# Kernel tuning notes

Hardware: AMD Instinct MI355X
Metric: run time of the kernel (lower is better)

Reference implementation:

```python
import jax, jax.numpy as jnp
import numpy as np

CH = 64
SCALE = 2
GROUPS = 4
K = 3
GN_GROUPS = min(CH // 8, 8)  # = 8
EPS_GN = 1e-5
EPS_COS = 1e-8


def setup_inputs() -> dict:
    key = jax.random.key(0)
    ks = jax.random.split(key, 4)
    B, H, W = 8, 256, 256
    OC = 2 * GROUPS
    lap = jnp.array([[0., -1., 0.], [-1., 4., -1.], [0., -1., 0.]], dtype=jnp.float32)
    hp_weight = jnp.tile(lap[None, None], (CH, 1, 1, 1))  # depthwise high-pass kernel
    return {
        "x": jax.random.normal(ks[0], (B, CH, H, W), dtype=jnp.float32),
        "gn_gamma": jnp.ones((CH,), jnp.float32),
        "gn_beta": jnp.zeros((CH,), jnp.float32),
        "hp_weight": hp_weight,
        "dir_w": jax.random.normal(ks[1], (OC, K * K - 1), jnp.float32) * 0.001,
        "dir_b": jnp.zeros((OC,), jnp.float32),
        "mag_w": jax.random.normal(ks[2], (OC, CH), jnp.float32) * 0.02,
        "mag_b": jnp.zeros((OC,), jnp.float32),
        "hfg_w": jax.random.normal(ks[3], (OC, CH), jnp.float32) * 0.02,
        "hfg_b": jnp.zeros((OC,), jnp.float32),
    }


def group_norm(x, gamma, beta, g, eps=EPS_GN):
    B, C, H, W = x.shape
    xr = x.reshape(B, g, -1)
    mu = xr.mean(-1, keepdims=True)
    var = xr.var(-1, keepdims=True)
    xn = ((xr - mu) * jax.lax.rsqrt(var + eps)).reshape(B, C, H, W)
    return xn * gamma[None, :, None, None] + beta[None, :, None, None]


def dw_conv3(x, w):
    # depthwise 3x3, padding=1, no bias
    return jax.lax.conv_general_dilated(
        x, w, window_strides=(1, 1), padding=((1, 1), (1, 1)),
        dimension_numbers=("NCHW", "OIHW", "NCHW"), feature_group_count=x.shape[1])


def avg_pool(x, s):
    B, C, H, W = x.shape
    return x.reshape(B, C, H // s, s, W // s, s).mean(axis=(3, 5))


def direction_feat(x, k=K):
    # cosine similarity (over channels) of center pixel vs each of k*k neighbors, center dropped
    B, C, H, W = x.shape
    p = k // 2
    xp = jnp.pad(x, ((0, 0), (0, 0), (p, p), (p, p)))
    patches = jnp.stack([xp[:, :, i:i + H, j:j + W]
                         for i in range(k) for j in range(k)], axis=2)  # [B,C,k2,H,W]
    center = patches[:, :, k * k // 2:k * k // 2 + 1]  # [B,C,1,H,W]
    dot = (center * patches).sum(axis=1)               # [B,k2,H,W]
    n1 = jnp.sqrt((center * center).sum(axis=1))       # [B,1,H,W]
    n2 = jnp.sqrt((patches * patches).sum(axis=1))     # [B,k2,H,W]
    sim = dot / (jnp.maximum(n1, EPS_COS) * jnp.maximum(n2, EPS_COS))
    c = k * k // 2
    return jnp.concatenate([sim[:, :c], sim[:, c + 1:]], axis=1)  # [B,k2-1,H,W]


def conv1x1(w, b, x):
    return jnp.einsum("oc,bchw->bohw", w, x) + b[None, :, None, None]


def grid_sample_border(x, grid):
    # x: [N,C,H,W]; grid: [N,Hg,Wg,2] in [-1,1]; bilinear, align_corners=False, padding_mode='border'
    N, C, H, W = x.shape
    gx, gy = grid[..., 0], grid[..., 1]
    ix = jnp.clip(((gx + 1.0) * W - 1.0) * 0.5, 0.0, W - 1.0)
    iy = jnp.clip(((gy + 1.0) * H - 1.0) * 0.5, 0.0, H - 1.0)
    x0 = jnp.floor(ix); y0 = jnp.floor(iy)
    wx = (ix - x0)[..., None]; wy = (iy - y0)[..., None]
    x0i = jnp.clip(x0.astype(jnp.int32), 0, W - 1)
    y0i = jnp.clip(y0.astype(jnp.int32), 0, H - 1)
    x1i = jnp.clip(x0i + 1, 0, W - 1)
    y1i = jnp.clip(y0i + 1, 0, H - 1)
    img = x.transpose(0, 2, 3, 1)  # [N,H,W,C]
    b = jnp.arange(N)[:, None, None]
    v00 = img[b, y0i, x0i]; v01 = img[b, y0i, x1i]
    v10 = img[b, y1i, x0i]; v11 = img[b, y1i, x1i]
    out = (v00 * (1 - wx) * (1 - wy) + v01 * wx * (1 - wy)
           + v10 * (1 - wx) * wy + v11 * wx * wy)
    return out.transpose(0, 3, 1, 2)  # [N,C,Hg,Wg]


def reference(x, gn_gamma, gn_beta, hp_weight, dir_w, dir_b, mag_w, mag_b, hfg_w, hfg_b):
    B, C, H, W = x.shape
    xn = group_norm(x, gn_gamma, gn_beta, GN_GROUPS)
    hf = dw_conv3(xn, hp_weight)
    xl = avg_pool(xn, SCALE)
    hfl = avg_pool(hf, SCALE)
    df = direction_feat(xl)
    gate = jax.nn.sigmoid(conv1x1(mag_w, mag_b, xl) + conv1x1(hfg_w, hfg_b, hfl))
    offset = conv1x1(dir_w, dir_b, df) * gate  # [B, 2*GROUPS, Hl, Wl]
    Hl, Wl = H // SCALE, W // SCALE
    off = offset.reshape(B, 2, GROUPS, Hl, Wl)
    cy = jnp.arange(Hl, dtype=x.dtype) * SCALE + SCALE / 2.0  # high-res pixel centers
    cx = jnp.arange(Wl, dtype=x.dtype) * SCALE + SCALE / 2.0
    gx = (cx[None, None, None, :] + off[:, 0]) * (2.0 / W) - 1.0  # [B,G,Hl,Wl]
    gy = (cy[None, None, :, None] + off[:, 1]) * (2.0 / H) - 1.0
    grid = jnp.stack([gx, gy], axis=-1).reshape(B * GROUPS, Hl, Wl, 2)
    xg = x.reshape(B * GROUPS, C // GROUPS, H, W)
    out = grid_sample_border(xg, grid)
    return out.reshape(B, C, Hl, Wl)
```

## Files before the change

### kernel.cpp

```cpp
#include <hip/hip_runtime.h>
#include <hip/hip_bf16.h>
#include <math.h>

#define B_ 8
#define C_ 64
#define H_ 256
#define W_ 256
#define HL_ 128
#define WL_ 128
#define GN_G 8
#define CPG 8
#define GRP 4
#define OC_ 8
#define GROUP_ELEMS (CPG * H_ * W_)

#define TILE_H 16
#define XROWS 34
#define LDSW 264

__global__ __launch_bounds__(256) void k2_fused(const float* __restrict__ x,
                                                const float* __restrict__ hpw,
                                                float* __restrict__ px,
                                                float* __restrict__ pL,
                                                float* __restrict__ partials) {
  __shared__ float tile[XROWS * LDSW];
  __shared__ float rs[4], rs2[4];
  const int t = threadIdx.x;
  const int blk = blockIdx.x;
  const int tileIdx = blk & 7;
  const int bc = blk >> 3;
  const int c = bc & 63;
  const int hl0 = tileIdx * TILE_H;
  const float* plane = x + (size_t)bc * (H_ * W_);
  const int y0 = 2 * hl0 - 1;

  if (t < XROWS * 2) {
    const int r = t >> 1;
    tile[r * LDSW + ((t & 1) ? 260 : 3)] = 0.f;
  }

  float s = 0.f, s2 = 0.f;
  for (int i = 0; i < 9; ++i) {
    const int q = t + i * 256;
    if (q >= XROWS * 64) break;
    const int r = q >> 6;
    const int c4 = (q & 63) << 2;
    const int y = y0 + r;
    float4 v = make_float4(0.f, 0.f, 0.f, 0.f);
    if ((unsigned)y < (unsigned)H_)
      v = *reinterpret_cast<const float4*>(plane + y * W_ + c4);
    *reinterpret_cast<float4*>(&tile[r * LDSW + 4 + c4]) = v;
    if (r >= 1 && r <= 32) {
      s  += v.x + v.y + v.z + v.w;
      s2 += v.x * v.x + v.y * v.y + v.z * v.z + v.w * v.w;
    }
  }
#pragma unroll
  for (int off = 32; off > 0; off >>= 1) {
    s  += __shfl_down(s, off, 64);
    s2 += __shfl_down(s2, off, 64);
  }
  if ((t & 63) == 0) { rs[t >> 6] = s; rs2[t >> 6] = s2; }
  __syncthreads();
  if (t == 0) {
    partials[blk * 2 + 0] = rs[0] + rs[1] + rs[2] + rs[3];
    partials[blk * 2 + 1] = rs2[0] + rs2[1] + rs2[2] + rs2[3];
  }

  float w[9];
#pragma unroll
  for (int i = 0; i < 9; ++i) w[i] = hpw[c * 9 + i];

  const int wl = t & 127;
  const int hs = (t >> 7) * 8;
  const int colb = 3 + 2 * wl;
  const int rbase = 2 * hs;
  float win[4][4];
#pragma unroll
  for (int j = 0; j < 4; ++j)
#pragma unroll
    for (int d = 0; d < 4; ++d)
      win[j][d] = tile[(rbase + j) * LDSW + colb + d];

  int outIdx = (bc * HL_ + (hl0 + hs)) * WL_ + wl;
#pragma unroll
  for (int i = 0; i < 8; ++i) {
    float pr[4][3];
#pragma unroll
    for (int j = 0; j < 4; ++j)
#pragma unroll
      for (int d = 0; d < 3; ++d) pr[j][d] = win[j][d] + win[j][d + 1];
    float hfsum = 0.f;
    float q11 = 0.f;
#pragma unroll
    for (int j = 0; j < 3; ++j)
#pragma unroll
      for (int d = 0; d < 3; ++d) {
        const float qq = pr[j][d] + pr[j + 1][d];
        hfsum = fmaf(w[j * 3 + d], qq, hfsum);
        if (j == 1 && d == 1) q11 = qq;
      }
    px[outIdx] = 0.25f * q11;
    pL[outIdx] = 0.25f * hfsum;
    outIdx += WL_;
    if (i < 7) {
      const int rn = rbase + 2 * i + 4;
#pragma unroll
      for (int d = 0; d < 4; ++d) {
        win[0][d] = win[2][d];
        win[1][d] = win[3][d];
        win[2][d] = tile[rn * LDSW + colb + d];
        win[3][d] = tile[(rn + 1) * LDSW + colb + d];
      }
    }
  }
}

__global__ __launch_bounds__(512) void k1_finish(const float* __restrict__ partials,
                                                 const float* __restrict__ gamma,
                                                 const float* __restrict__ beta,
                                                 float* __restrict__ ab) {
  const int t = threadIdx.x;
  const int b = t >> 6, c = t & 63, g = c >> 3;
  float S = 0.f, S2 = 0.f;
  for (int c2 = g * CPG; c2 < g * CPG + CPG; ++c2)
#pragma unroll
    for (int p = 0; p < 8; ++p) {
      const int blk = (b * 64 + c2) * 8 + p;
      S  += partials[blk * 2 + 0];
      S2 += partials[blk * 2 + 1];
    }
  const float N = (float)GROUP_ELEMS;
  const float mean = S / N;
  const float var = fmaxf(S2 / N - mean * mean, 0.f);
  const float a = rsqrtf(var + 1e-5f) * gamma[c];
  ab[t * 2 + 0] = a;
  ab[t * 2 + 1] = beta[c] - mean * a;
}

#define TS 16
__global__ __launch_bounds__(256) void k3_offset(const float* __restrict__ px,
                                                 const float* __restrict__ pL,
                                                 const float* __restrict__ ab,
                                                 const float* __restrict__ dir_w,
                                                 const float* __restrict__ dir_b,
                                                 const float* __restrict__ mag_w,
                                                 const float* __restrict__ mag_b,
                                                 const float* __restrict__ hfg_w,
                                                 const float* __restrict__ hfg_b,
                                                 float2* __restrict__ grid) {
  __shared__ float s_v[16][18][24];
  __shared__ float s_h[16][16][16];
  __shared__ float s_mw[C_][OC_];
  __shared__ float s_hw[C_][OC_];
  __shared__ float s_dir[OC_][8];
  __shared__ float s_ab2[C_][2];
  __shared__ float s_bias[2][OC_];

  const int tid = threadIdx.x;
  const int bx = blockIdx.x;
  const int tx = bx & 7, ty = (bx >> 3) & 7, b = bx >> 6;
  const int hl0 = ty * TS, wl0 = tx * TS;

  for (int i = tid; i < OC_ * C_; i += 256) {
    const int o = i >> 6, c = i & 63;
    s_mw[c][o] = mag_w[i];
    s_hw[c][o] = hfg_w[i];
  }
  if (tid < 64) s_dir[tid >> 3][tid & 7] = dir_w[tid];
  if (tid < 128) s_ab2[tid >> 1][tid & 1] = ab[b * 128 + tid];
  if (tid < OC_) { s_bias[0][tid] = mag_b[tid] + hfg_b[tid]; s_bias[1][tid] = dir_b[tid]; }

  const int pxi = tid & 15, pyi = tid >> 4;
  const int hl = hl0 + pyi, wl = wl0 + pxi;

  float dot[8], n2[8], z[8], n1 = 0.f;
#pragma unroll
  for (int k = 0; k < 8; ++k) { dot[k] = 0.f; n2[k] = 0.f; z[k] = 0.f; }

  const size_t planeSz = (size_t)HL_ * WL_;
  for (int cc = 0; cc < 4; ++cc) {
    __syncthreads();
    for (int q = tid; q < 16 * 18 * 6; q += 256) {
      const int c = q / 108, rem = q % 108, r = rem / 6, f4 = rem % 6;
      const int cg = cc * 16 + c;
      const int gy = hl0 - 1 + r;
      const int gx0 = wl0 - 4 + f4 * 4;
      const float a = s_ab2[cg][0], bb = s_ab2[cg][1];
      const float* pp = px + (size_t)(b * C_ + cg) * planeSz + gy * WL_ + gx0;
      float4 v = make_float4(0.f, 0.f, 0.f, 0.f);
      if ((unsigned)gy < (unsigned)HL_) {
        if (gx0 >= 0 && gx0 + 3 < WL_) {
          v = *reinterpret_cast<const float4*>(pp);
          v.x = fmaf(a, v.x, bb); v.y = fmaf(a, v.y, bb);
          v.z = fmaf(a, v.z, bb); v.w = fmaf(a, v.w, bb);
        } else {
          if ((unsigned)(gx0 + 0) < (unsigned)WL_) v.x = fmaf(a, pp[0], bb);
          if ((unsigned)(gx0 + 1) < (unsigned)WL_) v.y = fmaf(a, pp[1], bb);
          if ((unsigned)(gx0 + 2) < (unsigned)WL_) v.z = fmaf(a, pp[2], bb);
          if ((unsigned)(gx0 + 3) < (unsigned)WL_) v.w = fmaf(a, pp[3], bb);
        }
      }
      *reinterpret_cast<float4*>(&s_v[c][r][f4 * 4]) = v;
    }
    for (int q = tid; q < 16 * 16 * 4; q += 256) {
      const int c = q / 64, rem = q % 64, r = rem / 4, f4 = rem % 4;
      const int cg = cc * 16 + c;
      const int gy = hl0 + r, gx0 = wl0 + f4 * 4;
      const float a = s_ab2[cg][0], bb = s_ab2[cg][1];
      const float mh = (float)((gy == 0) + (gy == HL_ - 1));
      float4 v = *reinterpret_cast<const float4*>(pL + (size_t)(b * C_ + cg) * planeSz + gy * WL_ + gx0);
      v.x = fmaf(a, v.x, bb * 0.5f * (mh + (float)((gx0 + 0 == 0) + (gx0 + 0 == WL_ - 1))));
      v.y = fmaf(a, v.y, bb * 0.5f * (mh + (float)((gx0 + 1 == 0) + (gx0 + 1 == WL_ - 1))));
      v.z = fmaf(a, v.z, bb * 0.5f * (mh + (float)((gx0 + 2 == 0) + (gx0 + 2 == WL_ - 1))));
      v.w = fmaf(a, v.w, bb * 0.5f * (mh + (float)((gx0 + 3 == 0) + (gx0 + 3 == WL_ - 1))));
      *reinterpret_cast<float4*>(&s_h[c][r][f4 * 4]) = v;
    }
    __syncthreads();

#pragma unroll 2
    for (int c = 0; c < 16; ++c) {
      const int cg = cc * 16 + c;
      const float vc = s_v[c][pyi + 1][pxi + 4];
      const float vh = s_h[c][pyi][pxi];
      n1 = fmaf(vc, vc, n1);
      const float u0 = s_v[c][pyi][pxi + 3];
      const float u1 = s_v[c][pyi][pxi + 4];
      const float u2 = s_v[c][pyi][pxi + 5];
      const float u3 = s_v[c][pyi + 1][pxi + 3];
      const float u4 = s_v[c][pyi + 1][pxi + 5];
      const float u5 = s_v[c][pyi + 2][pxi + 3];
      const float u6 = s_v[c][pyi + 2][pxi + 4];
      const float u7 = s_v[c][pyi + 2][pxi + 5];
      dot[0] = fmaf(vc, u0, dot[0]); n2[0] = fmaf(u0, u0, n2[0]);
      dot[1] = fmaf(vc, u1, dot[1]); n2[1] = fmaf(u1, u1, n2[1]);
      dot[2] = fmaf(vc, u2, dot[2]); n2[2] = fmaf(u2, u2, n2[2]);
      dot[3] = fmaf(vc, u3, dot[3]); n2[3] = fmaf(u3, u3, n2[3]);
      dot[4] = fmaf(vc, u4, dot[4]); n2[4] = fmaf(u4, u4, n2[4]);
      dot[5] = fmaf(vc, u5, dot[5]); n2[5] = fmaf(u5, u5, n2[5]);
      dot[6] = fmaf(vc, u6, dot[6]); n2[6] = fmaf(u6, u6, n2[6]);
      dot[7] = fmaf(vc, u7, dot[7]); n2[7] = fmaf(u7, u7, n2[7]);
      const float4 mw0 = *reinterpret_cast<const float4*>(&s_mw[cg][0]);
      const float4 mw1 = *reinterpret_cast<const float4*>(&s_mw[cg][4]);
      const float4 hw0 = *reinterpret_cast<const float4*>(&s_hw[cg][0]);
      const float4 hw1 = *reinterpret_cast<const float4*>(&s_hw[cg][4]);
      z[0] = fmaf(mw0.x, vc, fmaf(hw0.x, vh, z[0]));
      z[1] = fmaf(mw0.y, vc, fmaf(hw0.y, vh, z[1]));
      z[2] = fmaf(mw0.z, vc, fmaf(hw0.z, vh, z[2]));
      z[3] = fmaf(mw0.w, vc, fmaf(hw0.w, vh, z[3]));
      z[4] = fmaf(mw1.x, vc, fmaf(hw1.x, vh, z[4]));
      z[5] = fmaf(mw1.y, vc, fmaf(hw1.y, vh, z[5]));
      z[6] = fmaf(mw1.z, vc, fmaf(hw1.z, vh, z[6]));
      z[7] = fmaf(mw1.w, vc, fmaf(hw1.w, vh, z[7]));
    }
  }

  const float n1c = fmaxf(sqrtf(n1), 1e-8f);
  float df[8];
#pragma unroll
  for (int k = 0; k < 8; ++k)
    df[k] = dot[k] / (n1c * fmaxf(sqrtf(n2[k]), 1e-8f));

  float off[8];
#pragma unroll
  for (int o = 0; o < 8; ++o) {
    float t1 = s_bias[1][o];
#pragma unroll
    for (int j = 0; j < 8; ++j) t1 = fmaf(s_dir[o][j], df[j], t1);
    const float zz = z[o] + s_bias[0][o];
    off[o] = t1 / (1.f + expf(-zz));
  }

#pragma unroll
  for (int g = 0; g < GRP; ++g) {
    const float ix = fminf(fmaxf(2.f * wl + 0.5f + off[g], 0.f), (float)(W_ - 1));
    const float iy = fminf(fmaxf(2.f * hl + 0.5f + off[GRP + g], 0.f), (float)(H_ - 1));
    grid[(b * GRP + g) * (HL_ * WL_) + hl * WL_ + wl] = make_float2(ix, iy);
  }
}

__global__ __launch_bounds__(256) void k4_sample(const float* __restrict__ x,
                                                 const float2* __restrict__ grid,
                                                 float* __restrict__ out) {
  const int idx = blockIdx.x * 256 + threadIdx.x;
  const int wl = idx & (WL_ - 1);
  const int hl = (idx >> 7) & (HL_ - 1);
  const int bc = idx >> 14;
  const int c = bc & 63;
  const int b = bc >> 6;
  const int g = c >> 4;
  const float2 G = grid[(b * GRP + g) * (HL_ * WL_) + hl * WL_ + wl];
  const float ix = G.x, iy = G.y;
  const float x0f = floorf(ix), y0f = floorf(iy);
  const float wx = ix - x0f, wy = iy - y0f;
  const int x0 = (int)x0f, y0 = (int)y0f;
  const int x1 = min(x0 + 1, W_ - 1), y1 = min(y0 + 1, H_ - 1);
  const float* plane = x + (size_t)bc * (H_ * W_);
  const float v00 = plane[y0 * W_ + x0];
  const float v01 = plane[y0 * W_ + x1];
  const float v10 = plane[y1 * W_ + x0];
  const float v11 = plane[y1 * W_ + x1];
  out[idx] = v00 * (1.f - wx) * (1.f - wy) + v01 * wx * (1.f - wy)
           + v10 * (1.f - wx) * wy + v11 * wx * wy;
}

extern "C" void kernel_launch(void* const* d_in, const int* in_sizes, int n_in,
                              void* d_out, int out_size, void* d_ws, size_t ws_size,
                              hipStream_t stream) {
  const float* x = (const float*)d_in[0];
  const float* gn_gamma = (const float*)d_in[1];
  const float* gn_beta = (const float*)d_in[2];
  const float* hp_weight = (const float*)d_in[3];
  const float* dir_w = (const float*)d_in[4];
  const float* dir_b = (const float*)d_in[5];
  const float* mag_w = (const float*)d_in[6];
  const float* mag_b = (const float*)d_in[7];
  const float* hfg_w = (const float*)d_in[8];
  const float* hfg_b = (const float*)d_in[9];
  float* out = (float*)d_out;

  float* ws = (float*)d_ws;
  float* partials = ws;
  float* ab = ws + 8192;
  float* px = ws + 16384;
  float* pL = px + (size_t)B_ * C_ * HL_ * WL_;
  float2* grid = (float2*)(pL + (size_t)B_ * C_ * HL_ * WL_);

  k2_fused<<<B_ * C_ * 8, 256, 0, stream>>>(x, hp_weight, px, pL, partials);
  k1_finish<<<1, 512, 0, stream>>>(partials, gn_gamma, gn_beta, ab);
  k3_offset<<<B_ * (HL_ / TS) * (WL_ / TS), 256, 0, stream>>>(px, pL, ab, dir_w, dir_b,
                                                              mag_w, mag_b, hfg_w, hfg_b, grid);
  k4_sample<<<(B_ * C_ * HL_ * WL_) / 256, 256, 0, stream>>>(x, grid, out);
}
```

Measured before the change: 111.7 us.

## Double-buffer k3 staging, read pL directly, and sample four channels per thread

In the offset kernel, the px halo tile is now double-buffered in shared memory, so the next channel chunk is staged while the current one is consumed. The pL tile is no longer staged through shared memory; each thread reads its own pL values directly and applies the affine and border correction in registers. The sampling kernel now has each thread handle four channels of one group, reusing a single grid load and the bilinear weights across them, and launches a quarter as many threads. The aim is to cut barrier stalls, shared-memory traffic and redundant grid loads, at the cost of more registers and a larger shared-memory footprint.

New measurement: 104.5 us. 1.07x faster.

```diff
diff --git a/kernel.cpp b/kernel.cpp
--- a/kernel.cpp
+++ b/kernel.cpp
@@ -149,8 +149,7 @@
                                                  const float* __restrict__ hfg_w,
                                                  const float* __restrict__ hfg_b,
                                                  float2* __restrict__ grid) {
-  __shared__ float s_v[16][18][24];
-  __shared__ float s_h[16][16][16];
+  __shared__ float s_v[2][16][18][24];
   __shared__ float s_mw[C_][OC_];
   __shared__ float s_hw[C_][OC_];
   __shared__ float s_dir[OC_][8];
@@ -161,6 +160,7 @@
   const int bx = blockIdx.x;
   const int tx = bx & 7, ty = (bx >> 3) & 7, b = bx >> 6;
   const int hl0 = ty * TS, wl0 = tx * TS;
+  const size_t planeSz = (size_t)HL_ * WL_;
 
   for (int i = tid; i < OC_ * C_; i += 256) {
     const int o = i >> 6, c = i & 63;
@@ -170,17 +170,9 @@
   if (tid < 64) s_dir[tid >> 3][tid & 7] = dir_w[tid];
   if (tid < 128) s_ab2[tid >> 1][tid & 1] = ab[b * 128 + tid];
   if (tid < OC_) { s_bias[0][tid] = mag_b[tid] + hfg_b[tid]; s_bias[1][tid] = dir_b[tid]; }
-
-  const int pxi = tid & 15, pyi = tid >> 4;
-  const int hl = hl0 + pyi, wl = wl0 + pxi;
-
-  float dot[8], n2[8], z[8], n1 = 0.f;
-#pragma unroll
-  for (int k = 0; k < 8; ++k) { dot[k] = 0.f; n2[k] = 0.f; z[k] = 0.f; }
-
-  const size_t planeSz = (size_t)HL_ * WL_;
-  for (int cc = 0; cc < 4; ++cc) {
-    __syncthreads();
+  __syncthreads();
+
+  auto stage = [&](int cc, int sel) {
     for (int q = tid; q < 16 * 18 * 6; q += 256) {
       const int c = q / 108, rem = q % 108, r = rem / 6, f4 = rem % 6;
       const int cg = cc * 16 + c;
@@ -201,37 +193,43 @@
           if ((unsigned)(gx0 + 3) < (unsigned)WL_) v.w = fmaf(a, pp[3], bb);
         }
       }
-      *reinterpret_cast<float4*>(&s_v[c][r][f4 * 4]) = v;
-    }
-    for (int q = tid; q < 16 * 16 * 4; q += 256) {
-      const int c = q / 64, rem = q % 64, r = rem / 4, f4 = rem % 4;
-      const int cg = cc * 16 + c;
-      const int gy = hl0 + r, gx0 = wl0 + f4 * 4;
-      const float a = s_ab2[cg][0], bb = s_ab2[cg][1];
-      const float mh = (float)((gy == 0) + (gy == HL_ - 1));
-      float4 v = *reinterpret_cast<const float4*>(pL + (size_t)(b * C_ + cg) * planeSz + gy * WL_ + gx0);
-      v.x = fmaf(a, v.x, bb * 0.5f * (mh + (float)((gx0 + 0 == 0) + (gx0 + 0 == WL_ - 1))));
-      v.y = fmaf(a, v.y, bb * 0.5f * (mh + (float)((gx0 + 1 == 0) + (gx0 + 1 == WL_ - 1))));
-      v.z = fmaf(a, v.z, bb * 0.5f * (mh + (float)((gx0 + 2 == 0) + (gx0 + 2 == WL_ - 1))));
-      v.w = fmaf(a, v.w, bb * 0.5f * (mh + (float)((gx0 + 3 == 0) + (gx0 + 3 == WL_ - 1))));
-      *reinterpret_cast<float4*>(&s_h[c][r][f4 * 4]) = v;
-    }
-    __syncthreads();
-
-#pragma unroll 2
+      *reinterpret_cast<float4*>(&s_v[sel][c][r][f4 * 4]) = v;
+    }
+  };
+
+  const int pxi = tid & 15, pyi = tid >> 4;
+  const int hl = hl0 + pyi, wl = wl0 + pxi;
+  const float mterm = 0.5f * ((hl == 0) + (hl == HL_ - 1) + (wl == 0) + (wl == WL_ - 1));
+
+  float dot[8], n2[8], z[8], n1 = 0.f;
+#pragma unroll
+  for (int k = 0; k < 8; ++k) { dot[k] = 0.f; n2[k] = 0.f; z[k] = 0.f; }
+
+  stage(0, 0);
+  __syncthreads();
+
+  for (int cc = 0; cc < 4; ++cc) {
+    if (cc < 3) stage(cc + 1, (cc + 1) & 1);
+    const int sel = cc & 1;
+    float lh[16];
+    const size_t pbase = (size_t)(b * C_ + cc * 16) * planeSz + hl * WL_ + wl;
+#pragma unroll
+    for (int c = 0; c < 16; ++c) lh[c] = pL[pbase + c * planeSz];
+#pragma unroll
     for (int c = 0; c < 16; ++c) {
       const int cg = cc * 16 + c;
-      const float vc = s_v[c][pyi + 1][pxi + 4];
-      const float vh = s_h[c][pyi][pxi];
+      const float a = s_ab2[cg][0], bb = s_ab2[cg][1];
+      const float vc = s_v[sel][c][pyi + 1][pxi + 4];
+      const float vh = fmaf(a, lh[c], bb * mterm);
       n1 = fmaf(vc, vc, n1);
-      const float u0 = s_v[c][pyi][pxi + 3];
-      const float u1 = s_v[c][pyi][pxi + 4];
-      const float u2 = s_v[c][pyi][pxi + 5];
-      const float u3 = s_v[c][pyi + 1][pxi + 3];
-      const float u4 = s_v[c][pyi + 1][pxi + 5];
-      const float u5 = s_v[c][pyi + 2][pxi + 3];
-      const float u6 = s_v[c][pyi + 2][pxi + 4];
-      const float u7 = s_v[c][pyi + 2][pxi + 5];
+      const float u0 = s_v[sel][c][pyi][pxi + 3];
+      const float u1 = s_v[sel][c][pyi][pxi + 4];
+      const float u2 = s_v[sel][c][pyi][pxi + 5];
+      const float u3 = s_v[sel][c][pyi + 1][pxi + 3];
+      const float u4 = s_v[sel][c][pyi + 1][pxi + 5];
+      const float u5 = s_v[sel][c][pyi + 2][pxi + 3];
+      const float u6 = s_v[sel][c][pyi + 2][pxi + 4];
+      const float u7 = s_v[sel][c][pyi + 2][pxi + 5];
       dot[0] = fmaf(vc, u0, dot[0]); n2[0] = fmaf(u0, u0, n2[0]);
       dot[1] = fmaf(vc, u1, dot[1]); n2[1] = fmaf(u1, u1, n2[1]);
       dot[2] = fmaf(vc, u2, dot[2]); n2[2] = fmaf(u2, u2, n2[2]);
@@ -253,6 +251,7 @@
       z[6] = fmaf(mw1.z, vc, fmaf(hw1.z, vh, z[6]));
       z[7] = fmaf(mw1.w, vc, fmaf(hw1.w, vh, z[7]));
     }
+    __syncthreads();
   }
 
   const float n1c = fmaxf(sqrtf(n1), 1e-8f);
@@ -285,23 +284,30 @@
   const int idx = blockIdx.x * 256 + threadIdx.x;
   const int wl = idx & (WL_ - 1);
   const int hl = (idx >> 7) & (HL_ - 1);
-  const int bc = idx >> 14;
-  const int c = bc & 63;
-  const int b = bc >> 6;
-  const int g = c >> 4;
+  const int qc = (idx >> 14) & 3;
+  const int g = (idx >> 16) & 3;
+  const int b = idx >> 18;
   const float2 G = grid[(b * GRP + g) * (HL_ * WL_) + hl * WL_ + wl];
   const float ix = G.x, iy = G.y;
   const float x0f = floorf(ix), y0f = floorf(iy);
   const float wx = ix - x0f, wy = iy - y0f;
   const int x0 = (int)x0f, y0 = (int)y0f;
   const int x1 = min(x0 + 1, W_ - 1), y1 = min(y0 + 1, H_ - 1);
-  const float* plane = x + (size_t)bc * (H_ * W_);
-  const float v00 = plane[y0 * W_ + x0];
-  const float v01 = plane[y0 * W_ + x1];
-  const float v10 = plane[y1 * W_ + x0];
-  const float v11 = plane[y1 * W_ + x1];
-  out[idx] = v00 * (1.f - wx) * (1.f - wy) + v01 * wx * (1.f - wy)
-           + v10 * (1.f - wx) * wy + v11 * wx * wy;
+  const float w00 = (1.f - wx) * (1.f - wy), w01 = wx * (1.f - wy);
+  const float w10 = (1.f - wx) * wy,        w11 = wx * wy;
+  const int c0 = g * 16 + qc * 4;
+  const float* plane = x + (size_t)(b * C_ + c0) * (H_ * W_);
+  float* po = out + (size_t)(b * C_ + c0) * (HL_ * WL_) + hl * WL_ + wl;
+#pragma unroll
+  for (int j = 0; j < 4; ++j) {
+    const float v00 = plane[y0 * W_ + x0];
+    const float v01 = plane[y0 * W_ + x1];
+    const float v10 = plane[y1 * W_ + x0];
+    const float v11 = plane[y1 * W_ + x1];
+    *po = fmaf(v00, w00, fmaf(v01, w01, fmaf(v10, w10, v11 * w11)));
+    plane += H_ * W_;
+    po += HL_ * WL_;
+  }
 }
 
 extern "C" void kernel_launch(void* const* d_in, const int* in_sizes, int n_in,
@@ -330,5 +336,5 @@
   k1_finish<<<1, 512, 0, stream>>>(partials, gn_gamma, gn_beta, ab);
   k3_offset<<<B_ * (HL_ / TS) * (WL_ / TS), 256, 0, stream>>>(px, pL, ab, dir_w, dir_b,
                                                               mag_w, mag_b, hfg_w, hfg_b, grid);
-  k4_sample<<<(B_ * C_ * HL_ * WL_) / 256, 256, 0, stream>>>(x, grid, out);
-}
+  k4_sample<<<(B_ * GRP * 4 * HL_ * WL_) / 256, 256, 0, stream>>>(x, grid, out);
+}
```
